# Optimization experiments

Hardware: AMD Instinct MI355X
Metric: run time of the kernel (lower is better)

The kernel has to match this reference:

```python
import jax, jax.numpy as jnp
import numpy as np

B, S, HID = 1, 2048, 2048
NH = 32
NOPE, ROPE = 128, 64
QK = NOPE + ROPE
VD = 128
KV_RANK = 512
SW = 128            # sliding window (layer_types[layer_idx] == 'sliding_attention')
SCALE = QK ** -0.5
NEG = -1e9


def rotate_half(x):
    h = x.shape[-1] // 2
    return jnp.concatenate([-x[..., h:], x[..., :h]], axis=-1)


def setup_inputs() -> dict:
    key = jax.random.key(0)
    ks = jax.random.split(key, 8)

    def n(k, shape, s=0.02):
        return jax.random.normal(k, shape, dtype=jnp.float32) * s

    hidden = jax.random.normal(ks[0], (B, S, HID), dtype=jnp.float32)
    # HF-style RoPE tables, broadcast to [B, S, ROPE]
    pos = jnp.arange(S, dtype=jnp.float32)
    inv = 1.0 / (10000.0 ** (jnp.arange(0, ROPE, 2, dtype=jnp.float32) / ROPE))
    ang = pos[:, None] * inv[None, :]
    ang = jnp.concatenate([ang, ang], axis=-1)
    cos = jnp.broadcast_to(jnp.cos(ang)[None], (B, S, ROPE))
    sin = jnp.broadcast_to(jnp.sin(ang)[None], (B, S, ROPE))
    return dict(
        hidden_states=hidden, cos=cos, sin=sin,
        Wq=n(ks[1], (HID, NH * QK)), bq=jnp.zeros((NH * QK,), jnp.float32),
        Wkva=n(ks[2], (HID, KV_RANK + ROPE)), bkva=jnp.zeros((KV_RANK + ROPE,), jnp.float32),
        Wkvb=n(ks[3], (KV_RANK, NH * (NOPE + VD))),
        Wo=n(ks[4], (NH * VD, HID)), bo=jnp.zeros((HID,), jnp.float32),
        sinks=jax.random.normal(ks[5], (NH,), dtype=jnp.float32),
    )


def reference(hidden_states, cos, sin, Wq, bq, Wkva, bkva, Wkvb, Wo, bo, sinks):
    b, s = hidden_states.shape[:2]
    # Q projection -> [b, nh, s, qk_head_dim]
    q = (hidden_states @ Wq + bq).reshape(b, s, NH, QK).transpose(0, 2, 1, 3)
    q_nope, q_rope = q[..., :NOPE], q[..., NOPE:]
    # MLA: compressed KV latent + shared (MQA) rope key
    ckv = hidden_states @ Wkva + bkva                       # [b, s, rank+rope]
    kv_lat, k_rope = ckv[..., :KV_RANK], ckv[..., KV_RANK:]
    kv = (kv_lat @ Wkvb).reshape(b, s, NH, NOPE + VD).transpose(0, 2, 1, 3)
    k_nope, v = kv[..., :NOPE], kv[..., NOPE:]              # [b, nh, s, *]
    k_rope = k_rope.reshape(b, 1, s, ROPE)                  # mla_rope_num_kv_heads = 1
    # RoPE (HF apply_rotary_pos_emb, unsqueeze head dim)
    c, si = cos[:, None], sin[:, None]
    q_rope = q_rope * c + rotate_half(q_rope) * si
    k_rope = k_rope * c + rotate_half(k_rope) * si
    k_rope = jnp.broadcast_to(k_rope, (b, NH, s, ROPE))     # repeat_kv
    qs = jnp.concatenate([q_nope, q_rope], axis=-1)
    kk = jnp.concatenate([k_nope, k_rope], axis=-1)
    # attention logits with causal + sliding-window mask
    logits = jnp.einsum('bhqd,bhkd->bhqk', qs, kk) * SCALE
    i = jnp.arange(s)[:, None]
    j = jnp.arange(s)[None, :]
    allowed = (j <= i) & (i - j < SW)
    logits = jnp.where(allowed[None, None], logits, NEG)
    # sink-augmented softmax: append learned per-head sink logit, softmax, drop it
    sink = jnp.broadcast_to(sinks[None, :, None, None], (b, NH, s, 1))
    probs = jax.nn.softmax(jnp.concatenate([logits, sink], axis=-1), axis=-1)[..., :-1]
    out = jnp.einsum('bhqk,bhkd->bhqd', probs, v)           # [b, nh, s, vd]
    out = out.transpose(0, 2, 1, 3).reshape(b, s, NH * VD)
    return out @ Wo + bo
```

## Files before the change

kernel.cpp:

```cpp
#include <hip/hip_runtime.h>
#include <hip/hip_bf16.h>
#include <math.h>

#define S_LEN 2048
#define HID_DIM 2048
#define NH 32
#define NOPE 128
#define ROPE_D 64
#define QKD 192
#define VD 128
#define KV_RANK 512
#define SW 128
#define NQK (NH*QKD)
#define CKV_N (KV_RANK+ROPE_D)
#define KVN (NH*(NOPE+VD))
#define KNW (NH*NOPE)
#define OUT_HID 2048
#define ATT_SCALE 0.07216878364870323f
#define NEG_INF (-1e30f)

typedef __bf16 bf16x8 __attribute__((ext_vector_type(8)));
typedef float  f32x4  __attribute__((ext_vector_type(4)));

__device__ __forceinline__ void async_load16(const void* gp, void* lp) {
    __builtin_amdgcn_global_load_lds(
        (const __attribute__((address_space(1))) void*)gp,
        (__attribute__((address_space(3))) void*)lp, 16, 0, 0);
}

__global__ __launch_bounds__(256)
void prep(const float* __restrict__ hidden, __hip_bfloat16* __restrict__ hid_bf,
          const float* __restrict__ Wq,   __hip_bfloat16* __restrict__ WqT,
          const float* __restrict__ Wkva, __hip_bfloat16* __restrict__ WkvaT,
          const float* __restrict__ Wo,   __hip_bfloat16* __restrict__ WoT)
{
    __shared__ float tile[64][65];
    int b = blockIdx.x;
    const int t = threadIdx.x;

    if (b < 4096) {
        int i = b * 256 + t;
        float4 v = ((const float4*)hidden)[i];
        hid_bf[i * 4 + 0] = __float2bfloat16(v.x);
        hid_bf[i * 4 + 1] = __float2bfloat16(v.y);
        hid_bf[i * 4 + 2] = __float2bfloat16(v.z);
        hid_bf[i * 4 + 3] = __float2bfloat16(v.w);
        return;
    }
    b -= 4096;
    const float* src; __hip_bfloat16* dst; int rows, cols, CX;
    if (b < 3072)               { src = Wq;   dst = WqT;   rows = 2048; cols = 6144; CX = 96; }
    else if ((b -= 3072) < 288) { src = Wkva; dst = WkvaT; rows = 2048; cols = 576;  CX = 9;  }
    else { b -= 288;              src = Wo;   dst = WoT;   rows = 4096; cols = 2048; CX = 32; }

    const int bx = b % CX, by = b / CX;
    const int r0 = by * 64, c0 = bx * 64;

    {
        const int r  = t >> 4;
        const int c4 = (t & 15) * 4;
        #pragma unroll
        for (int i = 0; i < 4; ++i) {
            const int rr = r + i * 16;
            float4 v = *(const float4*)&src[(size_t)(r0 + rr) * cols + c0 + c4];
            tile[rr][c4 + 0] = v.x;
            tile[rr][c4 + 1] = v.y;
            tile[rr][c4 + 2] = v.z;
            tile[rr][c4 + 3] = v.w;
        }
    }
    __syncthreads();
    const int tx = t & 63, ty = t >> 6;
    #pragma unroll
    for (int i = 0; i < 16; ++i) {
        const int dr = ty + i * 4;
        dst[(size_t)(c0 + dr) * rows + r0 + tx] = __float2bfloat16(tile[tx][dr]);
    }
}

#define BAR()   __builtin_amdgcn_s_barrier()
#define LGKM0() asm volatile("s_waitcnt lgkmcnt(0)" ::: "memory")
#define VMC(n)  asm volatile("s_waitcnt vmcnt(" #n ")" ::: "memory")

__device__ __forceinline__ void gemm256_core(
    const __hip_bfloat16* __restrict__ A, int lda,
    const __hip_bfloat16* __restrict__ Bt, int ldbt,
    int m0, int n0, int kbeg, int nit,
    __hip_bfloat16* lds, f32x4 (&acc)[8][4])
{
    const int t = threadIdx.x;
    const int w = t >> 6, L = t & 63;
    const int lane15 = L & 15, quad = L >> 4;
    const int wr = w >> 2, wc = w & 3;

    const int prw = w * 8 + (L >> 3);
    const int c8  = ((L & 7) ^ ((L >> 3) & 7)) * 8;
    const __hip_bfloat16* gA = A  + (size_t)(m0 + prw) * lda  + kbeg + c8;
    const __hip_bfloat16* gB = Bt + (size_t)(n0 + prw) * ldbt + kbeg + c8;
    const int uA = w * 512;
    const int uB = 16384 + w * 512;

    const int cx0 = ((quad)     ^ (L & 7)) * 8;
    const int cx1 = ((4 + quad) ^ (L & 7)) * 8;
    const int ra  = wr * 8192 + lane15 * 64;
    const int rb  = 16384 + (wc >> 1) * 8192 + (wc & 1) * 4096 + lane15 * 64;

    bf16x8 af[4][2], bfr[4][2];

    auto STG_A = [&](int buf, int h, int kt) {
        const __hip_bfloat16* g = gA + (size_t)h * 128 * lda + kt * 64;
        __hip_bfloat16* lp = lds + buf * 32768 + h * 8192 + uA;
        async_load16(g, lp);
        async_load16(g + (size_t)64 * lda, lp + 4096);
    };
    auto STG_B = [&](int buf, int h, int kt) {
        const __hip_bfloat16* g = gB + (size_t)h * 128 * ldbt + kt * 64;
        __hip_bfloat16* lp = lds + buf * 32768 + h * 8192 + uB;
        async_load16(g, lp);
        async_load16(g + (size_t)64 * ldbt, lp + 4096);
    };
    auto LDA4 = [&](int buf, int mlo) {
        const __hip_bfloat16* p0 = lds + buf * 32768 + ra;
        #pragma unroll
        for (int j = 0; j < 4; ++j) {
            af[j][0] = *(const bf16x8*)(const void*)(p0 + (mlo + j) * 1024 + cx0);
            af[j][1] = *(const bf16x8*)(const void*)(p0 + (mlo + j) * 1024 + cx1);
        }
    };
    auto LDB2 = [&](int buf, int nlo) {
        const __hip_bfloat16* p0 = lds + buf * 32768 + rb;
        #pragma unroll
        for (int n = 0; n < 2; ++n) {
            bfr[nlo + n][0] = *(const bf16x8*)(const void*)(p0 + (nlo + n) * 1024 + cx0);
            bfr[nlo + n][1] = *(const bf16x8*)(const void*)(p0 + (nlo + n) * 1024 + cx1);
        }
    };
    auto MMQ = [&](int mlo, int nlo) {
        __builtin_amdgcn_s_setprio(1);
        #pragma unroll
        for (int j = 0; j < 4; ++j)
            #pragma unroll
            for (int n = 0; n < 2; ++n)
                #pragma unroll
                for (int ks = 0; ks < 2; ++ks)
                    acc[mlo + j][nlo + n] = __builtin_amdgcn_mfma_f32_16x16x32_bf16(
                        af[j][ks], bfr[nlo + n][ks], acc[mlo + j][nlo + n], 0, 0, 0);
        __builtin_amdgcn_s_setprio(0);
    };

    STG_A(0, 0, 0); STG_B(0, 0, 0); STG_B(0, 1, 0); STG_A(0, 1, 0);
    STG_A(1, 0, 1); STG_B(1, 0, 1); STG_B(1, 1, 1);
    VMC(6);
    BAR();

    for (int it = 0; it < nit; ++it) {
        const int t0 = 2 * it, t1 = t0 + 1;
        const bool nl = (it + 1 < nit);
        LDA4(0, 0); LDB2(0, 0); STG_A(1, 1, t1);
        BAR(); LGKM0(); MMQ(0, 0); BAR();
        LDB2(0, 2);
        BAR(); LGKM0(); MMQ(0, 2); BAR();
        LDA4(0, 4); if (nl) STG_B(0, 0, t0 + 2);
        BAR(); LGKM0(); MMQ(4, 2); BAR();
        if (nl) { STG_B(0, 1, t0 + 2); STG_A(0, 0, t0 + 2); VMC(6); }
        else    { VMC(0); }
        BAR(); MMQ(4, 0); BAR();
        LDA4(1, 0); LDB2(1, 0); if (nl) STG_A(0, 1, t0 + 2);
        BAR(); LGKM0(); MMQ(0, 0); BAR();
        LDB2(1, 2);
        BAR(); LGKM0(); MMQ(0, 2); BAR();
        LDA4(1, 4); if (nl) STG_B(1, 0, t1 + 2);
        BAR(); LGKM0(); MMQ(4, 2); BAR();
        if (nl) { STG_B(1, 1, t1 + 2); STG_A(1, 0, t1 + 2); VMC(6); }
        BAR(); MMQ(4, 0); BAR();
    }
}

__global__ __launch_bounds__(512)
void gemm_q_ckv(const __hip_bfloat16* __restrict__ A,
                const __hip_bfloat16* __restrict__ BtQ,
                const __hip_bfloat16* __restrict__ BtKVA,
                const float* __restrict__ bq,
                const float* __restrict__ bkva,
                const float* __restrict__ cosb, const float* __restrict__ sinb,
                __hip_bfloat16* __restrict__ C,
                __hip_bfloat16* __restrict__ kvlat,
                __hip_bfloat16* __restrict__ kr,
                const float* __restrict__ Wkvb, __hip_bfloat16* __restrict__ WkvbT)
{
    __shared__ __hip_bfloat16 lds[65536];
    const int bid = blockIdx.x;
    const int t = threadIdx.x;

    if (bid >= 216) {
        float (*tile)[65] = (float (*)[65])(void*)lds;
        const int r  = t >> 4;
        const int c4 = (t & 15) * 4;
        const int tx = t & 63, ty = t >> 6;
        for (int id = bid - 216; id < 1024; id += 40) {
            const int bx = id & 127, by = id >> 7;
            const int r0 = by * 64, c0 = bx * 64;
            #pragma unroll
            for (int i = 0; i < 2; ++i) {
                const int rr = r + i * 32;
                float4 v = *(const float4*)&Wkvb[(size_t)(r0 + rr) * KVN + c0 + c4];
                tile[rr][c4 + 0] = v.x;
                tile[rr][c4 + 1] = v.y;
                tile[rr][c4 + 2] = v.z;
                tile[rr][c4 + 3] = v.w;
            }
            __syncthreads();
            #pragma unroll
            for (int i = 0; i < 8; ++i) {
                const int dr = ty + i * 8;
                WkvbT[(size_t)(c0 + dr) * KV_RANK + r0 + tx] = __float2bfloat16(tile[tx][dr]);
            }
            __syncthreads();
        }
        return;
    }

    const bool is_q = (bid < 192);
    const int m0 = (is_q ? (bid / 24) : ((bid - 192) / 3)) * 256;
    const int n0 = (is_q ? (bid % 24) : ((bid - 192) % 3)) * 256;

    f32x4 acc[8][4];
    #pragma unroll
    for (int mi = 0; mi < 8; ++mi)
        #pragma unroll
        for (int ni = 0; ni < 4; ++ni) acc[mi][ni] = (f32x4){0.f, 0.f, 0.f, 0.f};

    gemm256_core(A, HID_DIM, is_q ? BtQ : BtKVA, HID_DIM, m0, n0, 0,
                 HID_DIM / 128, lds, acc);

    const int w = t >> 6, L = t & 63;
    const int lane15 = L & 15, quad = L >> 4;
    const int wr = w >> 2, wc = w & 3;
    const int ns = n0 + wc * 64;

    if (is_q) {
        const bool do_rope = ((ns % 192) == 128);
        float bv[4];
        #pragma unroll
        for (int ni = 0; ni < 4; ++ni) bv[ni] = bq[ns + ni * 16 + lane15];

        #pragma unroll
        for (int mi = 0; mi < 8; ++mi) {
            const int rbase = m0 + wr * 128 + mi * 16 + quad * 4;
            float vv[4][4];
            #pragma unroll
            for (int ni = 0; ni < 4; ++ni)
                #pragma unroll
                for (int p = 0; p < 4; ++p) vv[ni][p] = acc[mi][ni][p] + bv[ni];
            if (do_rope) {
                #pragma unroll
                for (int ni = 0; ni < 2; ++ni) {
                    const int dd = ni * 16 + lane15;
                    #pragma unroll
                    for (int p = 0; p < 4; ++p) {
                        const int srow = rbase + p;
                        const float c0 = cosb[srow * ROPE_D + dd];
                        const float c1 = cosb[srow * ROPE_D + dd + 32];
                        const float s0 = sinb[srow * ROPE_D + dd];
                        const float s1 = sinb[srow * ROPE_D + dd + 32];
                        const float x0 = vv[ni][p], x1 = vv[ni + 2][p];
                        vv[ni][p]     = x0 * c0 - x1 * s0;
                        vv[ni + 2][p] = x1 * c1 + x0 * s1;
                    }
                }
            }
            #pragma unroll
            for (int ni = 0; ni < 4; ++ni) {
                const int c = ns + ni * 16 + lane15;
                #pragma unroll
                for (int p = 0; p < 4; ++p)
                    C[(size_t)(rbase + p) * NQK + c] = __float2bfloat16(vv[ni][p] * ATT_SCALE);
            }
        }
    } else if (ns < KV_RANK) {
        float bv[4];
        #pragma unroll
        for (int ni = 0; ni < 4; ++ni) bv[ni] = bkva[ns + ni * 16 + lane15];
        #pragma unroll
        for (int mi = 0; mi < 8; ++mi) {
            const int s = m0 + wr * 128 + mi * 16 + quad * 4;
            #pragma unroll
            for (int ni = 0; ni < 4; ++ni) {
                const int c = ns + ni * 16 + lane15;
                #pragma unroll
                for (int p = 0; p < 4; ++p)
                    kvlat[(size_t)(s + p) * KV_RANK + c] =
                        __float2bfloat16(acc[mi][ni][p] + bv[ni]);
            }
        }
    } else if (ns == KV_RANK) {
        #pragma unroll
        for (int mi = 0; mi < 8; ++mi) {
            const int sb = m0 + wr * 128 + mi * 16 + quad * 4;
            #pragma unroll
            for (int ni = 0; ni < 2; ++ni) {
                const int d = ni * 16 + lane15;
                const float ba = bkva[512 + d], bb = bkva[544 + d];
                #pragma unroll
                for (int p = 0; p < 4; ++p) {
                    const int s = sb + p;
                    const float a = acc[mi][ni][p] + ba;
                    const float b = acc[mi][ni + 2][p] + bb;
                    const float c0 = cosb[s * ROPE_D + d], c1 = cosb[s * ROPE_D + d + 32];
                    const float s0 = sinb[s * ROPE_D + d], s1 = sinb[s * ROPE_D + d + 32];
                    kr[(size_t)s * ROPE_D + d]      = __float2bfloat16(a * c0 - b * s0);
                    kr[(size_t)s * ROPE_D + d + 32] = __float2bfloat16(b * c1 + a * s1);
                }
            }
        }
    }
}

__global__ __launch_bounds__(512)
void gemm_kv256(const __hip_bfloat16* __restrict__ A,
                const __hip_bfloat16* __restrict__ Bt,
                __hip_bfloat16* __restrict__ kn,
                __hip_bfloat16* __restrict__ vt)
{
    __shared__ __hip_bfloat16 lds[65536];
    const int m0 = blockIdx.y * 256, n0 = blockIdx.x * 256;
    f32x4 acc[8][4];
    #pragma unroll
    for (int mi = 0; mi < 8; ++mi)
        #pragma unroll
        for (int ni = 0; ni < 4; ++ni) acc[mi][ni] = (f32x4){0.f, 0.f, 0.f, 0.f};

    gemm256_core(A, KV_RANK, Bt, KV_RANK, m0, n0, 0, KV_RANK / 128, lds, acc);

    const int t = threadIdx.x;
    const int w = t >> 6, L = t & 63;
    const int lane15 = L & 15, quad = L >> 4;
    const int wr = w >> 2, wc = w & 3;
    const int ns = n0 + wc * 64;

    #pragma unroll
    for (int mi = 0; mi < 8; ++mi) {
        const int rbase = m0 + wr * 128 + mi * 16 + quad * 4;
        #pragma unroll
        for (int ni = 0; ni < 4; ++ni) {
            const int c = ns + ni * 16 + lane15;
            const int h = c >> 8, d = c & 255;
            if (d < NOPE) {
                #pragma unroll
                for (int p = 0; p < 4; ++p)
                    kn[(size_t)(rbase + p) * KNW + h * NOPE + d] = __float2bfloat16(acc[mi][ni][p]);
            } else {
                ushort4 pk;
                __hip_bfloat16 b0 = __float2bfloat16(acc[mi][ni][0]);
                __hip_bfloat16 b1 = __float2bfloat16(acc[mi][ni][1]);
                __hip_bfloat16 b2 = __float2bfloat16(acc[mi][ni][2]);
                __hip_bfloat16 b3 = __float2bfloat16(acc[mi][ni][3]);
                pk.x = *(unsigned short*)&b0; pk.y = *(unsigned short*)&b1;
                pk.z = *(unsigned short*)&b2; pk.w = *(unsigned short*)&b3;
                *(ushort4*)(vt + (size_t)(h * VD + (d - NOPE)) * S_LEN + rbase) = pk;
            }
        }
    }
}

__global__ __launch_bounds__(512)
void gemm_partial256(const __hip_bfloat16* __restrict__ A, int lda,
                     const __hip_bfloat16* __restrict__ Bt, int ldbt,
                     float* __restrict__ P, int ldp, size_t zstride, int KL)
{
    __shared__ __hip_bfloat16 lds[65536];
    const int m0 = blockIdx.y * 256, n0 = blockIdx.x * 256;
    const int z  = blockIdx.z;
    f32x4 acc[8][4];
    #pragma unroll
    for (int mi = 0; mi < 8; ++mi)
        #pragma unroll
        for (int ni = 0; ni < 4; ++ni) acc[mi][ni] = (f32x4){0.f, 0.f, 0.f, 0.f};

    gemm256_core(A, lda, Bt, ldbt, m0, n0, z * KL, KL / 128, lds, acc);

    const int t = threadIdx.x;
    const int w = t >> 6, L = t & 63;
    const int lane15 = L & 15, quad = L >> 4;
    const int wr = w >> 2, wc = w & 3;
    float* Pz = P + (size_t)z * zstride;

    #pragma unroll
    for (int mi = 0; mi < 8; ++mi) {
        const int rbase = m0 + wr * 128 + mi * 16 + quad * 4;
        #pragma unroll
        for (int ni = 0; ni < 4; ++ni) {
            const int c = n0 + wc * 64 + ni * 16 + lane15;
            #pragma unroll
            for (int p = 0; p < 4; ++p)
                Pz[(size_t)(rbase + p) * ldp + c] = acc[mi][ni][p];
        }
    }
}

__global__ __launch_bounds__(256)
void wo_reduce4(const float* __restrict__ P, const float* __restrict__ bo,
                float* __restrict__ out)
{
    const size_t i = (size_t)blockIdx.x * 256 + threadIdx.x;
    const size_t zs = (size_t)S_LEN * OUT_HID;
    float4 a = ((const float4*)P)[i];
    float4 b = ((const float4*)(P + zs))[i];
    float4 c = ((const float4*)(P + 2 * zs))[i];
    float4 d = ((const float4*)(P + 3 * zs))[i];
    const int col = (int)((i * 4) & (OUT_HID - 1));
    float4 bb = *(const float4*)(bo + col);
    float4 o;
    o.x = a.x + b.x + c.x + d.x + bb.x;
    o.y = a.y + b.y + c.y + d.y + bb.y;
    o.z = a.z + b.z + c.z + d.z + bb.z;
    o.w = a.w + b.w + c.w + d.w + bb.w;
    ((float4*)out)[i] = o;
}

#define SS 170
#define SP 168
#define KSTR 200
#define VSTR 40

__global__ __launch_bounds__(256)
void attn_mfma2(const __hip_bfloat16* __restrict__ q,
                const __hip_bfloat16* __restrict__ kn,
                const __hip_bfloat16* __restrict__ kr,
                const __hip_bfloat16* __restrict__ vt,
                const float* __restrict__ sinks,
                __hip_bfloat16* __restrict__ out)
{
    __shared__ float lds_s[32 * SS];
    __shared__ __hip_bfloat16 lds_p[32 * SP];
    __shared__ __hip_bfloat16 lds_kv[32 * KSTR];

    const int h  = blockIdx.y;
    const int q0 = blockIdx.x * 32;
    const int t  = threadIdx.x;
    const int w  = t >> 6;
    const int L  = t & 63;
    const int lane15 = L & 15, quad = L >> 4;
    const int wm = (w & 1) * 16;
    const int wn = (w >> 1) * 16;

    int lo = q0 - SW + 1; if (lo < 0) lo = 0;
    const int cb = lo & ~31;
    const int nc = ((q0 - cb) >> 5) + 1;

    bf16x8 qf[6];
    {
        const __hip_bfloat16* qrow = q + (size_t)(q0 + wm + lane15) * NQK + h * QKD;
        #pragma unroll
        for (int kk = 0; kk < 6; ++kk)
            qf[kk] = *(const bf16x8*)(const void*)(qrow + kk * 32 + quad * 8);
    }

    for (int cc = 0; cc < nc; ++cc) {
        const int c0 = cb + cc * 32;
        __syncthreads();
        #pragma unroll
        for (int e = t; e < 768; e += 256) {
            const int row = e / 24, slot = e % 24;
            const int j = c0 + row;
            const __hip_bfloat16* g = (slot < 16)
                ? kn + (size_t)j * KNW + h * NOPE + slot * 8
                : kr + (size_t)j * ROPE_D + (slot - 16) * 8;
            *(bf16x8*)(void*)(lds_kv + row * KSTR + slot * 8) = *(const bf16x8*)(const void*)g;
        }
        __syncthreads();

        f32x4 s = (f32x4){0.f, 0.f, 0.f, 0.f};
        #pragma unroll
        for (int kk = 0; kk < 6; ++kk) {
            bf16x8 bf = *(const bf16x8*)(const void*)(lds_kv + (wn + lane15) * KSTR + kk * 32 + quad * 8);
            s = __builtin_amdgcn_mfma_f32_16x16x32_bf16(qf[kk], bf, s, 0, 0, 0);
        }
        const int j = c0 + wn + lane15;
        #pragma unroll
        for (int p = 0; p < 4; ++p) {
            const int i = q0 + wm + quad * 4 + p;
            const bool ok = (j <= i) && (i - j < SW);
            lds_s[(wm + quad * 4 + p) * SS + cc * 32 + wn + lane15] = ok ? s[p] : NEG_INF;
        }
    }
    __syncthreads();

    {
        const int r = t >> 3, g = t & 7;
        const int ncols = nc * 32;
        const float sink = sinks[h];
        float mx = sink;
        for (int c = g; c < ncols; c += 8)
            mx = fmaxf(mx, lds_s[r * SS + c]);
        #pragma unroll
        for (int off = 1; off < 8; off <<= 1)
            mx = fmaxf(mx, __shfl_xor(mx, off));
        float sum = 0.f;
        for (int c = g; c < ncols; c += 8) {
            float e = __expf(lds_s[r * SS + c] - mx);
            lds_s[r * SS + c] = e;
            sum += e;
        }
        #pragma unroll
        for (int off = 1; off < 8; off <<= 1)
            sum += __shfl_xor(sum, off);
        const float inv = 1.0f / (sum + __expf(sink - mx));
        for (int c = g; c < ncols; c += 8)
            lds_p[r * SP + c] = __float2bfloat16(lds_s[r * SS + c] * inv);
    }

    f32x4 oacc[4];
    #pragma unroll
    for (int ni = 0; ni < 4; ++ni) oacc[ni] = (f32x4){0.f, 0.f, 0.f, 0.f};

    for (int cc = 0; cc < nc; ++cc) {
        const int c0 = cb + cc * 32;
        __syncthreads();
        #pragma unroll
        for (int e = t; e < 512; e += 256) {
            const int row = e >> 2, slot = e & 3;
            *(bf16x8*)(void*)(lds_kv + row * VSTR + slot * 8) =
                *(const bf16x8*)(const void*)(vt + (size_t)(h * VD + row) * S_LEN + c0 + slot * 8);
        }
        __syncthreads();

        bf16x8 ap = *(const bf16x8*)(const void*)(lds_p + (wm + lane15) * SP + cc * 32 + quad * 8);
        #pragma unroll
        for (int ni = 0; ni < 4; ++ni) {
            bf16x8 bv = *(const bf16x8*)(const void*)(lds_kv + ((w >> 1) * 64 + ni * 16 + lane15) * VSTR + quad * 8);
            oacc[ni] = __builtin_amdgcn_mfma_f32_16x16x32_bf16(ap, bv, oacc[ni], 0, 0, 0);
        }
    }

    #pragma unroll
    for (int ni = 0; ni < 4; ++ni) {
        const int col = h * VD + (w >> 1) * 64 + ni * 16 + lane15;
        #pragma unroll
        for (int p = 0; p < 4; ++p) {
            const int row = q0 + wm + quad * 4 + p;
            out[(size_t)row * (NH * VD) + col] = __float2bfloat16(oacc[ni][p]);
        }
    }
}

extern "C" void kernel_launch(void* const* d_in, const int* in_sizes, int n_in,
                              void* d_out, int out_size, void* d_ws, size_t ws_size,
                              hipStream_t stream) {
    const float* hidden = (const float*)d_in[0];
    const float* cosb   = (const float*)d_in[1];
    const float* sinb   = (const float*)d_in[2];
    const float* Wq     = (const float*)d_in[3];
    const float* bq     = (const float*)d_in[4];
    const float* Wkva   = (const float*)d_in[5];
    const float* bkva   = (const float*)d_in[6];
    const float* Wkvb   = (const float*)d_in[7];
    const float* Wo     = (const float*)d_in[8];
    const float* bo     = (const float*)d_in[9];
    const float* sinks  = (const float*)d_in[10];
    float* out = (float*)d_out;

    uint8_t* p = (uint8_t*)d_ws;
    __hip_bfloat16* attn_bf = (__hip_bfloat16*)p; p += (size_t)S_LEN * NH * VD * 2;
    __hip_bfloat16* WoT     = (__hip_bfloat16*)p; p += (size_t)OUT_HID * (NH*VD) * 2;
    __hip_bfloat16* q_bf    = (__hip_bfloat16*)p; p += (size_t)S_LEN * NQK * 2;
    __hip_bfloat16* hid_bf  = (__hip_bfloat16*)p; p += (size_t)S_LEN * HID_DIM * 2;
    __hip_bfloat16* WqT     = (__hip_bfloat16*)p; p += (size_t)NQK * HID_DIM * 2;
    __hip_bfloat16* WkvaT   = (__hip_bfloat16*)p; p += (size_t)640 * HID_DIM * 2;
    __hip_bfloat16* WkvbT   = (__hip_bfloat16*)p; p += (size_t)KVN * KV_RANK * 2;
    __hip_bfloat16* kn_bf   = (__hip_bfloat16*)p; p += (size_t)S_LEN * KNW * 2;
    __hip_bfloat16* vt_bf   = (__hip_bfloat16*)p; p += (size_t)S_LEN * NH * VD * 2;
    __hip_bfloat16* kr_bf   = (__hip_bfloat16*)p; p += (size_t)S_LEN * ROPE_D * 2;
    __hip_bfloat16* kvlat   = (__hip_bfloat16*)p; p += (size_t)S_LEN * KV_RANK * 2;
    float* WoP = (float*)q_bf;

    prep<<<9504, 256, 0, stream>>>(hidden, hid_bf, Wq, WqT, Wkva, WkvaT, Wo, WoT);

    gemm_q_ckv<<<256, 512, 0, stream>>>(
        hid_bf, WqT, WkvaT, bq, bkva, cosb, sinb, q_bf, kvlat, kr_bf,
        Wkvb, WkvbT);

    gemm_kv256<<<dim3(KVN / 256, S_LEN / 256), 512, 0, stream>>>(
        kvlat, WkvbT, kn_bf, vt_bf);

    attn_mfma2<<<dim3(S_LEN / 32, NH), 256, 0, stream>>>(
        q_bf, kn_bf, kr_bf, vt_bf, sinks, attn_bf);

    gemm_partial256<<<dim3(OUT_HID / 256, S_LEN / 256, 4), 512, 0, stream>>>(
        attn_bf, NH * VD, WoT, NH * VD, WoP, OUT_HID, (size_t)S_LEN * OUT_HID, 1024);

    wo_reduce4<<<(S_LEN * OUT_HID / 4) / 256, 256, 0, stream>>>(WoP, bo, out);
}
```

Measured before the change: 343.6 us.

## Register-prefetch K/V chunks in attention and vectorize transpose stores

```diff
diff --git a/kernel.cpp b/kernel.cpp
--- a/kernel.cpp
+++ b/kernel.cpp
@@ -70,11 +70,21 @@
         }
     }
     __syncthreads();
-    const int tx = t & 63, ty = t >> 6;
-    #pragma unroll
-    for (int i = 0; i < 16; ++i) {
-        const int dr = ty + i * 4;
-        dst[(size_t)(c0 + dr) * rows + r0 + tx] = __float2bfloat16(tile[tx][dr]);
+    {
+        const int tx0 = (t & 15) * 4;
+        const int drb = t >> 4;
+        #pragma unroll
+        for (int i = 0; i < 4; ++i) {
+            const int dr = drb + i * 16;
+            __hip_bfloat16 b0 = __float2bfloat16(tile[tx0 + 0][dr]);
+            __hip_bfloat16 b1 = __float2bfloat16(tile[tx0 + 1][dr]);
+            __hip_bfloat16 b2 = __float2bfloat16(tile[tx0 + 2][dr]);
+            __hip_bfloat16 b3 = __float2bfloat16(tile[tx0 + 3][dr]);
+            ushort4 pk;
+            pk.x = *(unsigned short*)&b0; pk.y = *(unsigned short*)&b1;
+            pk.z = *(unsigned short*)&b2; pk.w = *(unsigned short*)&b3;
+            *(ushort4*)&dst[(size_t)(c0 + dr) * rows + r0 + tx0] = pk;
+        }
     }
 }
 
@@ -196,7 +206,8 @@
         float (*tile)[65] = (float (*)[65])(void*)lds;
         const int r  = t >> 4;
         const int c4 = (t & 15) * 4;
-        const int tx = t & 63, ty = t >> 6;
+        const int tx0 = (t & 15) * 4;
+        const int drb = t >> 4;
         for (int id = bid - 216; id < 1024; id += 40) {
             const int bx = id & 127, by = id >> 7;
             const int r0 = by * 64, c0 = bx * 64;
@@ -211,9 +222,16 @@
             }
             __syncthreads();
             #pragma unroll
-            for (int i = 0; i < 8; ++i) {
-                const int dr = ty + i * 8;
-                WkvbT[(size_t)(c0 + dr) * KV_RANK + r0 + tx] = __float2bfloat16(tile[tx][dr]);
+            for (int i = 0; i < 2; ++i) {
+                const int dr = drb + i * 32;
+                __hip_bfloat16 b0 = __float2bfloat16(tile[tx0 + 0][dr]);
+                __hip_bfloat16 b1 = __float2bfloat16(tile[tx0 + 1][dr]);
+                __hip_bfloat16 b2 = __float2bfloat16(tile[tx0 + 2][dr]);
+                __hip_bfloat16 b3 = __float2bfloat16(tile[tx0 + 3][dr]);
+                ushort4 pk;
+                pk.x = *(unsigned short*)&b0; pk.y = *(unsigned short*)&b1;
+                pk.z = *(unsigned short*)&b2; pk.w = *(unsigned short*)&b3;
+                *(ushort4*)&WkvbT[(size_t)(c0 + dr) * KV_RANK + r0 + tx0] = pk;
             }
             __syncthreads();
         }
@@ -448,26 +466,60 @@
     const int cb = lo & ~31;
     const int nc = ((q0 - cb) >> 5) + 1;
 
-    bf16x8 qf[6];
-    {
-        const __hip_bfloat16* qrow = q + (size_t)(q0 + wm + lane15) * NQK + h * QKD;
-        #pragma unroll
-        for (int kk = 0; kk < 6; ++kk)
-            qf[kk] = *(const bf16x8*)(const void*)(qrow + kk * 32 + quad * 8);
-    }
-
-    for (int cc = 0; cc < nc; ++cc) {
-        const int c0 = cb + cc * 32;
-        __syncthreads();
-        #pragma unroll
-        for (int e = t; e < 768; e += 256) {
+    bf16x8 kreg[3];
+    auto issueK = [&](int c0) {
+        #pragma unroll
+        for (int i = 0; i < 3; ++i) {
+            const int e = t + i * 256;
             const int row = e / 24, slot = e % 24;
             const int j = c0 + row;
             const __hip_bfloat16* g = (slot < 16)
                 ? kn + (size_t)j * KNW + h * NOPE + slot * 8
                 : kr + (size_t)j * ROPE_D + (slot - 16) * 8;
-            *(bf16x8*)(void*)(lds_kv + row * KSTR + slot * 8) = *(const bf16x8*)(const void*)g;
-        }
+            kreg[i] = *(const bf16x8*)(const void*)g;
+        }
+    };
+    auto writeK = [&]() {
+        #pragma unroll
+        for (int i = 0; i < 3; ++i) {
+            const int e = t + i * 256;
+            const int row = e / 24, slot = e % 24;
+            *(bf16x8*)(void*)(lds_kv + row * KSTR + slot * 8) = kreg[i];
+        }
+    };
+    bf16x8 vreg[2];
+    auto issueV = [&](int c0) {
+        #pragma unroll
+        for (int i = 0; i < 2; ++i) {
+            const int e = t + i * 256;
+            const int row = e >> 2, slot = e & 3;
+            vreg[i] = *(const bf16x8*)(const void*)(
+                vt + (size_t)(h * VD + row) * S_LEN + c0 + slot * 8);
+        }
+    };
+    auto writeV = [&]() {
+        #pragma unroll
+        for (int i = 0; i < 2; ++i) {
+            const int e = t + i * 256;
+            const int row = e >> 2, slot = e & 3;
+            *(bf16x8*)(void*)(lds_kv + row * VSTR + slot * 8) = vreg[i];
+        }
+    };
+
+    bf16x8 qf[6];
+    {
+        const __hip_bfloat16* qrow = q + (size_t)(q0 + wm + lane15) * NQK + h * QKD;
+        #pragma unroll
+        for (int kk = 0; kk < 6; ++kk)
+            qf[kk] = *(const bf16x8*)(const void*)(qrow + kk * 32 + quad * 8);
+    }
+
+    issueK(cb);
+    for (int cc = 0; cc < nc; ++cc) {
+        const int c0 = cb + cc * 32;
+        __syncthreads();
+        writeK();
+        if (cc + 1 < nc) issueK(cb + (cc + 1) * 32);
         __syncthreads();
 
         f32x4 s = (f32x4){0.f, 0.f, 0.f, 0.f};
@@ -485,6 +537,8 @@
         }
     }
     __syncthreads();
+
+    issueV(cb);
 
     {
         const int r = t >> 3, g = t & 7;
@@ -515,14 +569,9 @@
     for (int ni = 0; ni < 4; ++ni) oacc[ni] = (f32x4){0.f, 0.f, 0.f, 0.f};
 
     for (int cc = 0; cc < nc; ++cc) {
-        const int c0 = cb + cc * 32;
         __syncthreads();
-        #pragma unroll
-        for (int e = t; e < 512; e += 256) {
-            const int row = e >> 2, slot = e & 3;
-            *(bf16x8*)(void*)(lds_kv + row * VSTR + slot * 8) =
-                *(const bf16x8*)(const void*)(vt + (size_t)(h * VD + row) * S_LEN + c0 + slot * 8);
-        }
+        writeV();
+        if (cc + 1 < nc) issueV(cb + (cc + 1) * 32);
         __syncthreads();
 
         bf16x8 ap = *(const bf16x8*)(const void*)(lds_p + (wm + lane15) * SP + cc * 32 + quad * 8);
```

After: 334.0 us. 2.8% less time.
